# Optimization experiments

Measured on AMD Instinct MI355X. Metric: run time of the kernel, lower is better.

The kernel has to match this reference:

```python
import jax, jax.numpy as jnp
import numpy as np

EMBED_DIM = 192
NUM_HEADS = 4
HEAD_DIM = EMBED_DIM // NUM_HEADS
SCALE = HEAD_DIM ** -0.5


def setup_inputs() -> dict:
    key = jax.random.key(0)
    k_x, k_wqkv, k_bqkv, k_wp, k_bp = jax.random.split(key, 5)
    B, P, N, d = 8, 4, 1024, EMBED_DIM
    x = jax.random.normal(k_x, (B, P, N, d), dtype=jnp.float32)
    # torch Linear: y = x @ W.T + b, W shape [out, in]
    w_qkv = jax.random.normal(k_wqkv, (3 * d, d), dtype=jnp.float32) * (d ** -0.5)
    b_qkv = jax.random.normal(k_bqkv, (3 * d,), dtype=jnp.float32) * 0.02
    w_proj = jax.random.normal(k_wp, (d, d), dtype=jnp.float32) * (d ** -0.5)
    b_proj = jax.random.normal(k_bp, (d,), dtype=jnp.float32) * 0.02
    return {"x": x, "w_qkv": w_qkv, "b_qkv": b_qkv, "w_proj": w_proj, "b_proj": b_proj}


def reference(x, w_qkv, b_qkv, w_proj, b_proj):
    B, P, N, d = x.shape
    H, D = NUM_HEADS, HEAD_DIM
    qkv = jnp.einsum('bpnd,ed->bpne', x, w_qkv) + b_qkv  # [B,P,N,3d]
    q, k, v = jnp.split(qkv, 3, axis=-1)
    # split heads -> [B,P,H,N,D]
    split = lambda t: t.reshape(B, P, N, H, D).transpose(0, 1, 3, 2, 4)
    q, k, v = split(q), split(k), split(v)
    attn = jnp.einsum('bphnd,bphmd->bphnm', q, k) * SCALE
    attn = jax.nn.softmax(attn, axis=-1)
    z = jnp.einsum('bphnm,bphmd->bphnd', attn, v)
    z = z.transpose(0, 1, 3, 2, 4).reshape(B, P, N, H * D)
    z = jnp.einsum('bpnd,ed->bpne', z, w_proj) + b_proj
    return z
```

## Files before the change

### kernel.cpp

```cpp
#include <hip/hip_runtime.h>
#include <hip/hip_bf16.h>
#include <cstdint>
#include <cstddef>

typedef __attribute__((ext_vector_type(8))) short bf16x8;
typedef __attribute__((ext_vector_type(4))) float floatx4;
typedef __attribute__((ext_vector_type(16))) float floatx16;

#define SCALE_L2E 0.20823560929138437f

#define BPH 128
#define SEQ 1024
#define DMODEL 192
#define DHEAD 48
#define MROWS 32768
#define RESCALE_THR 11.5f

#define ZERO16 {0.f,0.f,0.f,0.f,0.f,0.f,0.f,0.f,0.f,0.f,0.f,0.f,0.f,0.f,0.f,0.f}

__device__ __forceinline__ unsigned short bfu(float f) {
    return __bfloat16_as_ushort(__float2bfloat16(f));
}
__device__ __forceinline__ unsigned pk2(float lo, float hi) {
    return (unsigned)bfu(lo) | ((unsigned)bfu(hi) << 16);
}

__global__ __launch_bounds__(256) void qkv_kernel(
    const float* __restrict__ x,
    const float* __restrict__ w_qkv,
    const float* __restrict__ b_qkv,
    unsigned short* __restrict__ q_ws,
    unsigned short* __restrict__ k_ws,
    unsigned short* __restrict__ vt_ws)
{
    __shared__ unsigned short a_lds[64 * 200];
    __shared__ unsigned short w_lds[64 * 200];
    const int t = threadIdx.x;
    const int m0 = blockIdx.x * 64;
    const int n0 = blockIdx.y * 64;

    #pragma unroll
    for (int i = 0; i < 12; ++i) {
        int idx = t + i * 256;
        int row = idx / 48, c4 = idx % 48;
        float4 v = *reinterpret_cast<const float4*>(x + (size_t)(m0 + row) * DMODEL + c4 * 4);
        unsigned short* dst = &a_lds[row * 200 + c4 * 4];
        dst[0] = bfu(v.x); dst[1] = bfu(v.y); dst[2] = bfu(v.z); dst[3] = bfu(v.w);
    }
    #pragma unroll
    for (int i = 0; i < 12; ++i) {
        int idx = t + i * 256;
        int row = idx / 48, c4 = idx % 48;
        float4 v = *reinterpret_cast<const float4*>(w_qkv + (size_t)(n0 + row) * DMODEL + c4 * 4);
        unsigned short* dst = &w_lds[row * 200 + c4 * 4];
        dst[0] = bfu(v.x); dst[1] = bfu(v.y); dst[2] = bfu(v.z); dst[3] = bfu(v.w);
    }
    __syncthreads();

    const int lane = t & 63, w = t >> 6;
    const int lrow = lane & 15, lhi = lane >> 4;

    floatx4 zf = {0.f, 0.f, 0.f, 0.f};
    floatx4 acc[4] = {zf, zf, zf, zf};

    #pragma unroll
    for (int ks = 0; ks < 6; ++ks) {
        bf16x8 af = *reinterpret_cast<const bf16x8*>(&a_lds[(w * 16 + lrow) * 200 + ks * 32 + lhi * 8]);
        #pragma unroll
        for (int cb = 0; cb < 4; ++cb) {
            bf16x8 bfr = *reinterpret_cast<const bf16x8*>(&w_lds[(cb * 16 + lrow) * 200 + ks * 32 + lhi * 8]);
            acc[cb] = __builtin_amdgcn_mfma_f32_16x16x32_bf16(af, bfr, acc[cb], 0, 0, 0);
        }
    }

    const int sec = n0 / 192;
    if (sec == 2) {
        __syncthreads();
        #pragma unroll
        for (int cb = 0; cb < 4; ++cb) {
            float bias = b_qkv[n0 + cb * 16 + lrow];
            #pragma unroll
            for (int r = 0; r < 4; ++r)
                a_lds[(cb * 16 + lrow) * 72 + (w * 16 + lhi * 4 + r)] = bfu(acc[cb][r] + bias);
        }
        __syncthreads();
        const int bp = m0 >> 10, nb = m0 & 1023;
        #pragma unroll
        for (int i = 0; i < 2; ++i) {
            int ch = t + i * 256;
            int c_local = ch >> 3, seg = ch & 7;
            int cc = n0 + c_local - 384;
            int h = cc / 48, dd = cc - h * 48;
            *reinterpret_cast<bf16x8*>(
                &vt_ws[((size_t)(bp * 4 + h) * DHEAD + dd) * SEQ + nb + seg * 8]) =
                *reinterpret_cast<const bf16x8*>(&a_lds[c_local * 72 + seg * 8]);
        }
    } else {
        #pragma unroll
        for (int cb = 0; cb < 4; ++cb) {
            int c = n0 + cb * 16 + lrow;
            int cc = c - sec * 192;
            int h = cc / 48, dd = cc - h * 48;
            float bias = b_qkv[c];
            #pragma unroll
            for (int r = 0; r < 4; ++r) {
                int m = m0 + w * 16 + lhi * 4 + r;
                float val = acc[cb][r] + bias;
                int bp = m >> 10, n = m & 1023;
                int bph = bp * 4 + h;
                if (sec == 0) {
                    q_ws[((size_t)bph * SEQ + n) * DHEAD + dd] = bfu(val * SCALE_L2E);
                } else {
                    k_ws[((size_t)bph * SEQ + n) * DHEAD + dd] = bfu(val);
                }
            }
        }
    }
}

__global__ __launch_bounds__(256, 4) void attn_kernel(
    const unsigned short* __restrict__ q_ws,
    const unsigned short* __restrict__ k_ws,
    const unsigned short* __restrict__ vt_ws,
    unsigned short* __restrict__ z_ws)
{
    const int t = threadIdx.x, lane = t & 63, w = t >> 6;
    const int q31 = lane & 31, hi = lane >> 5;
    const int d = blockIdx.x;
    const int bph = (d & 7) | ((d >> 6) << 3);
    const int qc = (d >> 3) & 7;
    const int q0 = qc * 128 + w * 32;
    const int bp = bph >> 2, h = bph & 3;

    bf16x8 qf[3];
    {
        const unsigned short* qp = q_ws + ((size_t)bph * SEQ + q0 + q31) * DHEAD + hi * 8;
        #pragma unroll
        for (int ks = 0; ks < 3; ++ks)
            qf[ks] = *reinterpret_cast<const bf16x8*>(qp + ks * 16);
    }

    const unsigned short* kp  = k_ws + ((size_t)bph * SEQ + q31) * DHEAD + hi * 8;
    const int vrow1 = (32 + q31 > 47) ? 47 : (32 + q31);
    const unsigned short* vp0 = vt_ws + ((size_t)bph * DHEAD + q31)  * (size_t)SEQ + hi * 8;
    const unsigned short* vp1 = vt_ws + ((size_t)bph * DHEAD + vrow1) * (size_t)SEQ + hi * 8;

    floatx16 oa0 = ZERO16, oa1 = ZERO16;
    float m_prev = -INFINITY, l_sum = 0.f;

    #pragma unroll 1
    for (int kt = 0; kt < 16; ++kt) {
        const int kt0 = kt * 64;

        const unsigned short* kpt = kp + (size_t)kt0 * DHEAD;
        bf16x8 kf[6], vf0[4], vf1[4];
        #pragma unroll
        for (int ks = 0; ks < 3; ++ks) {
            kf[ks]     = *reinterpret_cast<const bf16x8*>(kpt + ks * 16);
            kf[ks + 3] = *reinterpret_cast<const bf16x8*>(kpt + 32 * DHEAD + ks * 16);
        }
        #pragma unroll
        for (int ksv = 0; ksv < 4; ++ksv) {
            vf0[ksv] = *reinterpret_cast<const bf16x8*>(vp0 + kt0 + ksv * 16);
            vf1[ksv] = *reinterpret_cast<const bf16x8*>(vp1 + kt0 + ksv * 16);
        }

        floatx16 s0 = ZERO16, s1 = ZERO16;
        #pragma unroll
        for (int ks = 0; ks < 3; ++ks) {
            s0 = __builtin_amdgcn_mfma_f32_32x32x16_bf16(kf[ks],     qf[ks], s0, 0, 0, 0);
            s1 = __builtin_amdgcn_mfma_f32_32x32x16_bf16(kf[ks + 3], qf[ks], s1, 0, 0, 0);
        }

        float tmax = fmaxf(s0[0], s1[0]);
        #pragma unroll
        for (int r = 1; r < 16; ++r) tmax = fmaxf(tmax, fmaxf(s0[r], s1[r]));
        tmax = fmaxf(tmax, __shfl_xor(tmax, 32, 64));
        if (!__all((int)(tmax <= m_prev + RESCALE_THR))) {
            const float mnew = fmaxf(m_prev, tmax);
            const float scale = exp2f(m_prev - mnew);
            m_prev = mnew;
            l_sum *= scale;
            oa0 = oa0 * scale;
            oa1 = oa1 * scale;
        }
        const float mref = m_prev;

        float ts = 0.f;
        #pragma unroll
        for (int kvb = 0; kvb < 2; ++kvb) {
            unsigned W[8], X[8];
            #pragma unroll
            for (int u = 0; u < 8; ++u) {
                float e0 = __builtin_amdgcn_exp2f((kvb ? s1[2*u]   : s0[2*u])   - mref);
                float e1 = __builtin_amdgcn_exp2f((kvb ? s1[2*u+1] : s0[2*u+1]) - mref);
                ts += e0 + e1;
                W[u] = pk2(e0, e1);
                X[u] = __shfl_xor(W[u], 32, 64);
            }
            #pragma unroll
            for (int s = 0; s < 2; ++s) {
                const int a = s * 4;
                union { bf16x8 v; unsigned wd[4]; } pf;
                pf.wd[0] = hi ? X[a+2] : W[a];
                pf.wd[1] = hi ? X[a+3] : W[a+1];
                pf.wd[2] = hi ? W[a+2] : X[a];
                pf.wd[3] = hi ? W[a+3] : X[a+1];
                const int ksv = kvb * 2 + s;
                oa0 = __builtin_amdgcn_mfma_f32_32x32x16_bf16(vf0[ksv], pf.v, oa0, 0, 0, 0);
                oa1 = __builtin_amdgcn_mfma_f32_32x32x16_bf16(vf1[ksv], pf.v, oa1, 0, 0, 0);
            }
        }
        ts += __shfl_xor(ts, 32, 64);
        l_sum += ts;
    }

    const float inv = 1.0f / l_sum;
    unsigned* zp = reinterpret_cast<unsigned*>(
        z_ws + ((size_t)bp * SEQ + q0 + q31) * DMODEL + h * DHEAD);
    #pragma unroll
    for (int u = 0; u < 8; ++u) {
        int dd = 2 * (u & 1) + 8 * (u >> 1) + 4 * hi;
        zp[dd >> 1] = pk2(oa0[2*u] * inv, oa0[2*u+1] * inv);
    }
    #pragma unroll
    for (int u = 0; u < 4; ++u) {
        int dd = 32 + 2 * (u & 1) + 8 * (u >> 1) + 4 * hi;
        zp[dd >> 1] = pk2(oa1[2*u] * inv, oa1[2*u+1] * inv);
    }
}

__global__ __launch_bounds__(256) void proj_kernel(
    const unsigned short* __restrict__ z_ws,
    const float* __restrict__ w_proj,
    const float* __restrict__ b_proj,
    float* __restrict__ out)
{
    __shared__ unsigned short a_lds[64 * 200];
    __shared__ unsigned short w_lds[64 * 200];
    const int t = threadIdx.x;
    const int m0 = blockIdx.x * 64;
    const int n0 = blockIdx.y * 64;

    for (int i = t; i < 1536; i += 256) {
        int row = i / 24, c8 = i % 24;
        *reinterpret_cast<bf16x8*>(&a_lds[row * 200 + c8 * 8]) =
            *reinterpret_cast<const bf16x8*>(&z_ws[(size_t)(m0 + row) * DMODEL + c8 * 8]);
    }
    #pragma unroll
    for (int i = 0; i < 12; ++i) {
        int idx = t + i * 256;
        int row = idx / 48, c4 = idx % 48;
        float4 v = *reinterpret_cast<const float4*>(w_proj + (size_t)(n0 + row) * DMODEL + c4 * 4);
        unsigned short* dst = &w_lds[row * 200 + c4 * 4];
        dst[0] = bfu(v.x); dst[1] = bfu(v.y); dst[2] = bfu(v.z); dst[3] = bfu(v.w);
    }
    __syncthreads();

    const int lane = t & 63, w = t >> 6;
    const int lrow = lane & 15, lhi = lane >> 4;

    floatx4 zf = {0.f, 0.f, 0.f, 0.f};
    floatx4 acc[4] = {zf, zf, zf, zf};

    #pragma unroll
    for (int ks = 0; ks < 6; ++ks) {
        bf16x8 af = *reinterpret_cast<const bf16x8*>(&a_lds[(w * 16 + lrow) * 200 + ks * 32 + lhi * 8]);
        #pragma unroll
        for (int cb = 0; cb < 4; ++cb) {
            bf16x8 bfr = *reinterpret_cast<const bf16x8*>(&w_lds[(cb * 16 + lrow) * 200 + ks * 32 + lhi * 8]);
            acc[cb] = __builtin_amdgcn_mfma_f32_16x16x32_bf16(af, bfr, acc[cb], 0, 0, 0);
        }
    }

    #pragma unroll
    for (int cb = 0; cb < 4; ++cb) {
        int c = n0 + cb * 16 + lrow;
        float bias = b_proj[c];
        #pragma unroll
        for (int r = 0; r < 4; ++r) {
            int m = m0 + w * 16 + lhi * 4 + r;
            out[(size_t)m * DMODEL + c] = acc[cb][r] + bias;
        }
    }
}

extern "C" void kernel_launch(void* const* d_in, const int* in_sizes, int n_in,
                              void* d_out, int out_size, void* d_ws, size_t ws_size,
                              hipStream_t stream) {
    const float* x      = (const float*)d_in[0];
    const float* w_qkv  = (const float*)d_in[1];
    const float* b_qkv  = (const float*)d_in[2];
    const float* w_proj = (const float*)d_in[3];
    const float* b_proj = (const float*)d_in[4];
    float* out = (float*)d_out;

    unsigned short* q_ws  = (unsigned short*)d_ws;
    unsigned short* k_ws  = q_ws  + (size_t)BPH * SEQ * DHEAD;
    unsigned short* vt_ws = k_ws  + (size_t)BPH * SEQ * DHEAD;
    unsigned short* z_ws  = vt_ws + (size_t)BPH * DHEAD * SEQ;

    qkv_kernel<<<dim3(512, 9), 256, 0, stream>>>(x, w_qkv, b_qkv, q_ws, k_ws, vt_ws);
    attn_kernel<<<1024, 256, 0, stream>>>(q_ws, k_ws, vt_ws, z_ws);
    proj_kernel<<<dim3(512, 3), 256, 0, stream>>>(z_ws, w_proj, b_proj, out);
}
```

Measured before the change: 111.1 us.

## Stage K/V tiles through double-buffered LDS via async global-to-LDS loads

```diff
diff --git a/kernel.cpp b/kernel.cpp
--- a/kernel.cpp
+++ b/kernel.cpp
@@ -6,6 +6,7 @@
 typedef __attribute__((ext_vector_type(8))) short bf16x8;
 typedef __attribute__((ext_vector_type(4))) float floatx4;
 typedef __attribute__((ext_vector_type(16))) float floatx16;
+typedef __attribute__((ext_vector_type(2))) unsigned uintx2;
 
 #define SCALE_L2E 0.20823560929138437f
 
@@ -23,6 +24,12 @@
 }
 __device__ __forceinline__ unsigned pk2(float lo, float hi) {
     return (unsigned)bfu(lo) | ((unsigned)bfu(hi) << 16);
+}
+__device__ __forceinline__ void gload16(const unsigned short* g, unsigned short* l) {
+    __builtin_amdgcn_global_load_lds(
+        (const __attribute__((address_space(1))) unsigned int*)g,
+        (__attribute__((address_space(3))) unsigned int*)l,
+        16, 0, 0);
 }
 
 __global__ __launch_bounds__(256) void qkv_kernel(
@@ -44,16 +51,16 @@
         int idx = t + i * 256;
         int row = idx / 48, c4 = idx % 48;
         float4 v = *reinterpret_cast<const float4*>(x + (size_t)(m0 + row) * DMODEL + c4 * 4);
-        unsigned short* dst = &a_lds[row * 200 + c4 * 4];
-        dst[0] = bfu(v.x); dst[1] = bfu(v.y); dst[2] = bfu(v.z); dst[3] = bfu(v.w);
+        uintx2 p; p.x = pk2(v.x, v.y); p.y = pk2(v.z, v.w);
+        *reinterpret_cast<uintx2*>(&a_lds[row * 200 + c4 * 4]) = p;
     }
     #pragma unroll
     for (int i = 0; i < 12; ++i) {
         int idx = t + i * 256;
         int row = idx / 48, c4 = idx % 48;
         float4 v = *reinterpret_cast<const float4*>(w_qkv + (size_t)(n0 + row) * DMODEL + c4 * 4);
-        unsigned short* dst = &w_lds[row * 200 + c4 * 4];
-        dst[0] = bfu(v.x); dst[1] = bfu(v.y); dst[2] = bfu(v.z); dst[3] = bfu(v.w);
+        uintx2 p; p.x = pk2(v.x, v.y); p.y = pk2(v.z, v.w);
+        *reinterpret_cast<uintx2*>(&w_lds[row * 200 + c4 * 4]) = p;
     }
     __syncthreads();
 
@@ -124,6 +131,9 @@
     const unsigned short* __restrict__ vt_ws,
     unsigned short* __restrict__ z_ws)
 {
+    __shared__ unsigned short k_lds[2][384 * 8];
+    __shared__ unsigned short v_lds[2][384 * 8];
+
     const int t = threadIdx.x, lane = t & 63, w = t >> 6;
     const int q31 = lane & 31, hi = lane >> 5;
     const int d = blockIdx.x;
@@ -132,50 +142,85 @@
     const int q0 = qc * 128 + w * 32;
     const int bp = bph >> 2, h = bph & 3;
 
+    const size_t kbase = (size_t)bph * SEQ;
+    const size_t vbase = (size_t)bph * DHEAD;
+
+    const unsigned short* s0p = k_ws + (kbase + (t & 63)) * 48 + (t >> 6) * 8;
+    const unsigned short* s1p;
+    size_t step1;
+    int c1;
+    const bool c1k = (t < 128);
+    if (c1k) {
+        c1 = t + 256;
+        s1p = k_ws + (kbase + (c1 & 63)) * 48 + (c1 >> 6) * 8;
+        step1 = 48;
+    } else {
+        c1 = t - 128;
+        int vkhi = c1 / 48, dd = c1 - vkhi * 48;
+        s1p = vt_ws + (vbase + dd) * SEQ + vkhi * 8;
+        step1 = 1;
+    }
+    const int c2 = t + 128;
+    const int vkhi2 = c2 / 48, dd2 = c2 - vkhi2 * 48;
+    const unsigned short* s2p = vt_ws + (vbase + dd2) * SEQ + vkhi2 * 8;
+
     bf16x8 qf[3];
     {
-        const unsigned short* qp = q_ws + ((size_t)bph * SEQ + q0 + q31) * DHEAD + hi * 8;
+        const unsigned short* qp = q_ws + (kbase + q0 + q31) * DHEAD + hi * 8;
         #pragma unroll
         for (int ks = 0; ks < 3; ++ks)
             qf[ks] = *reinterpret_cast<const bf16x8*>(qp + ks * 16);
     }
 
-    const unsigned short* kp  = k_ws + ((size_t)bph * SEQ + q31) * DHEAD + hi * 8;
-    const int vrow1 = (32 + q31 > 47) ? 47 : (32 + q31);
-    const unsigned short* vp0 = vt_ws + ((size_t)bph * DHEAD + q31)  * (size_t)SEQ + hi * 8;
-    const unsigned short* vp1 = vt_ws + ((size_t)bph * DHEAD + vrow1) * (size_t)SEQ + hi * 8;
+    const int vrow1m = (32 + q31 > 47) ? 47 : (32 + q31);
 
     floatx16 oa0 = ZERO16, oa1 = ZERO16;
     float m_prev = -INFINITY, l_sum = 0.f;
 
+    gload16(s0p, &k_lds[0][t * 8]);
+    gload16(s1p, c1k ? &k_lds[0][c1 * 8] : &v_lds[0][c1 * 8]);
+    gload16(s2p, &v_lds[0][c2 * 8]);
+    __syncthreads();
+
     #pragma unroll 1
     for (int kt = 0; kt < 16; ++kt) {
-        const int kt0 = kt * 64;
-
-        const unsigned short* kpt = kp + (size_t)kt0 * DHEAD;
+        const int cur = kt & 1;
+        if (kt < 15) {
+            const size_t kt0n = (size_t)(kt + 1) * 64;
+            gload16(s0p + kt0n * 48,   &k_lds[cur ^ 1][t * 8]);
+            gload16(s1p + kt0n * step1, c1k ? &k_lds[cur ^ 1][c1 * 8] : &v_lds[cur ^ 1][c1 * 8]);
+            gload16(s2p + kt0n,        &v_lds[cur ^ 1][c2 * 8]);
+        }
+
+        const unsigned short* kb = k_lds[cur];
+        const unsigned short* vb = v_lds[cur];
+
         bf16x8 kf[6], vf0[4], vf1[4];
         #pragma unroll
         for (int ks = 0; ks < 3; ++ks) {
-            kf[ks]     = *reinterpret_cast<const bf16x8*>(kpt + ks * 16);
-            kf[ks + 3] = *reinterpret_cast<const bf16x8*>(kpt + 32 * DHEAD + ks * 16);
+            kf[ks]     = *reinterpret_cast<const bf16x8*>(&kb[((ks * 2 + hi) * 64 + q31) * 8]);
+            kf[ks + 3] = *reinterpret_cast<const bf16x8*>(&kb[((ks * 2 + hi) * 64 + q31 + 32) * 8]);
         }
         #pragma unroll
         for (int ksv = 0; ksv < 4; ++ksv) {
-            vf0[ksv] = *reinterpret_cast<const bf16x8*>(vp0 + kt0 + ksv * 16);
-            vf1[ksv] = *reinterpret_cast<const bf16x8*>(vp1 + kt0 + ksv * 16);
+            vf0[ksv] = *reinterpret_cast<const bf16x8*>(&vb[((ksv * 2 + hi) * 48 + q31) * 8]);
+            vf1[ksv] = *reinterpret_cast<const bf16x8*>(&vb[((ksv * 2 + hi) * 48 + vrow1m) * 8]);
         }
 
         floatx16 s0 = ZERO16, s1 = ZERO16;
+        __builtin_amdgcn_s_setprio(1);
         #pragma unroll
         for (int ks = 0; ks < 3; ++ks) {
             s0 = __builtin_amdgcn_mfma_f32_32x32x16_bf16(kf[ks],     qf[ks], s0, 0, 0, 0);
             s1 = __builtin_amdgcn_mfma_f32_32x32x16_bf16(kf[ks + 3], qf[ks], s1, 0, 0, 0);
         }
+        __builtin_amdgcn_s_setprio(0);
 
         float tmax = fmaxf(s0[0], s1[0]);
         #pragma unroll
         for (int r = 1; r < 16; ++r) tmax = fmaxf(tmax, fmaxf(s0[r], s1[r]));
         tmax = fmaxf(tmax, __shfl_xor(tmax, 32, 64));
+
         if (!__all((int)(tmax <= m_prev + RESCALE_THR))) {
             const float mnew = fmaxf(m_prev, tmax);
             const float scale = exp2f(m_prev - mnew);
@@ -187,6 +232,8 @@
         const float mref = m_prev;
 
         float ts = 0.f;
+        union U { bf16x8 v; unsigned wd[4]; };
+        __builtin_amdgcn_s_setprio(1);
         #pragma unroll
         for (int kvb = 0; kvb < 2; ++kvb) {
             unsigned W[8], X[8];
@@ -201,7 +248,7 @@
             #pragma unroll
             for (int s = 0; s < 2; ++s) {
                 const int a = s * 4;
-                union { bf16x8 v; unsigned wd[4]; } pf;
+                U pf;
                 pf.wd[0] = hi ? X[a+2] : W[a];
                 pf.wd[1] = hi ? X[a+3] : W[a+1];
                 pf.wd[2] = hi ? W[a+2] : X[a];
@@ -211,8 +258,11 @@
                 oa1 = __builtin_amdgcn_mfma_f32_32x32x16_bf16(vf1[ksv], pf.v, oa1, 0, 0, 0);
             }
         }
+        __builtin_amdgcn_s_setprio(0);
         ts += __shfl_xor(ts, 32, 64);
         l_sum += ts;
+
+        __syncthreads();
     }
 
     const float inv = 1.0f / l_sum;
@@ -252,8 +302,8 @@
         int idx = t + i * 256;
         int row = idx / 48, c4 = idx % 48;
         float4 v = *reinterpret_cast<const float4*>(w_proj + (size_t)(n0 + row) * DMODEL + c4 * 4);
-        unsigned short* dst = &w_lds[row * 200 + c4 * 4];
-        dst[0] = bfu(v.x); dst[1] = bfu(v.y); dst[2] = bfu(v.z); dst[3] = bfu(v.w);
+        uintx2 p; p.x = pk2(v.x, v.y); p.y = pk2(v.z, v.w);
+        *reinterpret_cast<uintx2*>(&w_lds[row * 200 + c4 * 4]) = p;
     }
     __syncthreads();
 
```

New measurement: 119.1 us. 1.07x slower.

## Use P-as-A-operand 32x32x8 MFMA with blocked V layout to drop shuffles

Applied to the files above, without the earlier changes.

```diff
diff --git a/kernel.cpp b/kernel.cpp
--- a/kernel.cpp
+++ b/kernel.cpp
@@ -4,8 +4,10 @@
 #include <cstddef>
 
 typedef __attribute__((ext_vector_type(8))) short bf16x8;
+typedef __attribute__((ext_vector_type(4))) short bf16x4;
 typedef __attribute__((ext_vector_type(4))) float floatx4;
 typedef __attribute__((ext_vector_type(16))) float floatx16;
+typedef __attribute__((ext_vector_type(2))) unsigned uintx2;
 
 #define SCALE_L2E 0.20823560929138437f
 
@@ -15,6 +17,7 @@
 #define DHEAD 48
 #define MROWS 32768
 #define RESCALE_THR 11.5f
+#define VSTRIDE 49152
 
 #define ZERO16 {0.f,0.f,0.f,0.f,0.f,0.f,0.f,0.f,0.f,0.f,0.f,0.f,0.f,0.f,0.f,0.f}
 
@@ -24,6 +27,17 @@
 __device__ __forceinline__ unsigned pk2(float lo, float hi) {
     return (unsigned)bfu(lo) | ((unsigned)bfu(hi) << 16);
 }
+
+#if __has_builtin(__builtin_amdgcn_mfma_f32_32x32x8bf16_1k)
+__device__ __forceinline__ floatx16 mfma8(bf16x4 a, bf16x4 b, floatx16 c) {
+    return __builtin_amdgcn_mfma_f32_32x32x8bf16_1k(a, b, c, 0, 0, 0);
+}
+#else
+__device__ __forceinline__ floatx16 mfma8(bf16x4 a, bf16x4 b, floatx16 c) {
+    asm("v_mfma_f32_32x32x8_bf16 %0, %1, %2, %0" : "+v"(c) : "v"(a), "v"(b));
+    return c;
+}
+#endif
 
 __global__ __launch_bounds__(256) void qkv_kernel(
     const float* __restrict__ x,
@@ -31,7 +45,7 @@
     const float* __restrict__ b_qkv,
     unsigned short* __restrict__ q_ws,
     unsigned short* __restrict__ k_ws,
-    unsigned short* __restrict__ vt_ws)
+    unsigned short* __restrict__ v2_ws)
 {
     __shared__ unsigned short a_lds[64 * 200];
     __shared__ unsigned short w_lds[64 * 200];
@@ -44,16 +58,16 @@
         int idx = t + i * 256;
         int row = idx / 48, c4 = idx % 48;
         float4 v = *reinterpret_cast<const float4*>(x + (size_t)(m0 + row) * DMODEL + c4 * 4);
-        unsigned short* dst = &a_lds[row * 200 + c4 * 4];
-        dst[0] = bfu(v.x); dst[1] = bfu(v.y); dst[2] = bfu(v.z); dst[3] = bfu(v.w);
+        uintx2 p; p.x = pk2(v.x, v.y); p.y = pk2(v.z, v.w);
+        *reinterpret_cast<uintx2*>(&a_lds[row * 200 + c4 * 4]) = p;
     }
     #pragma unroll
     for (int i = 0; i < 12; ++i) {
         int idx = t + i * 256;
         int row = idx / 48, c4 = idx % 48;
         float4 v = *reinterpret_cast<const float4*>(w_qkv + (size_t)(n0 + row) * DMODEL + c4 * 4);
-        unsigned short* dst = &w_lds[row * 200 + c4 * 4];
-        dst[0] = bfu(v.x); dst[1] = bfu(v.y); dst[2] = bfu(v.z); dst[3] = bfu(v.w);
+        uintx2 p; p.x = pk2(v.x, v.y); p.y = pk2(v.z, v.w);
+        *reinterpret_cast<uintx2*>(&w_lds[row * 200 + c4 * 4]) = p;
     }
     __syncthreads();
 
@@ -92,7 +106,7 @@
             int cc = n0 + c_local - 384;
             int h = cc / 48, dd = cc - h * 48;
             *reinterpret_cast<bf16x8*>(
-                &vt_ws[((size_t)(bp * 4 + h) * DHEAD + dd) * SEQ + nb + seg * 8]) =
+                &v2_ws[(size_t)(bp * 4 + h) * VSTRIDE + (size_t)(nb / 8 + seg) * 384 + dd * 8]) =
                 *reinterpret_cast<const bf16x8*>(&a_lds[c_local * 72 + seg * 8]);
         }
     } else {
@@ -121,7 +135,7 @@
 __global__ __launch_bounds__(256, 4) void attn_kernel(
     const unsigned short* __restrict__ q_ws,
     const unsigned short* __restrict__ k_ws,
-    const unsigned short* __restrict__ vt_ws,
+    const unsigned short* __restrict__ v2_ws,
     unsigned short* __restrict__ z_ws)
 {
     const int t = threadIdx.x, lane = t & 63, w = t >> 6;
@@ -140,93 +154,96 @@
             qf[ks] = *reinterpret_cast<const bf16x8*>(qp + ks * 16);
     }
 
-    const unsigned short* kp  = k_ws + ((size_t)bph * SEQ + q31) * DHEAD + hi * 8;
-    const int vrow1 = (32 + q31 > 47) ? 47 : (32 + q31);
-    const unsigned short* vp0 = vt_ws + ((size_t)bph * DHEAD + q31)  * (size_t)SEQ + hi * 8;
-    const unsigned short* vp1 = vt_ws + ((size_t)bph * DHEAD + vrow1) * (size_t)SEQ + hi * 8;
+    const unsigned short* kp = k_ws + ((size_t)bph * SEQ + q31) * DHEAD + hi * 8;
+    const int dB = 32 + (q31 < 16 ? q31 : 15);
+    const unsigned short* vpA = v2_ws + (size_t)bph * VSTRIDE + q31 * 8 + hi * 4;
+    const unsigned short* vpB = v2_ws + (size_t)bph * VSTRIDE + dB  * 8 + hi * 4;
 
     floatx16 oa0 = ZERO16, oa1 = ZERO16;
     float m_prev = -INFINITY, l_sum = 0.f;
 
     #pragma unroll 1
     for (int kt = 0; kt < 16; ++kt) {
-        const int kt0 = kt * 64;
-
-        const unsigned short* kpt = kp + (size_t)kt0 * DHEAD;
-        bf16x8 kf[6], vf0[4], vf1[4];
+        const unsigned short* kpt = kp + (size_t)kt * 64 * DHEAD;
+        bf16x8 kf[6];
         #pragma unroll
         for (int ks = 0; ks < 3; ++ks) {
             kf[ks]     = *reinterpret_cast<const bf16x8*>(kpt + ks * 16);
             kf[ks + 3] = *reinterpret_cast<const bf16x8*>(kpt + 32 * DHEAD + ks * 16);
         }
-        #pragma unroll
-        for (int ksv = 0; ksv < 4; ++ksv) {
-            vf0[ksv] = *reinterpret_cast<const bf16x8*>(vp0 + kt0 + ksv * 16);
-            vf1[ksv] = *reinterpret_cast<const bf16x8*>(vp1 + kt0 + ksv * 16);
+        bf16x4 vA[8], vB[8];
+        const size_t vto = (size_t)kt * 3072;
+        #pragma unroll
+        for (int j = 0; j < 8; ++j) {
+            vA[j] = *reinterpret_cast<const bf16x4*>(vpA + vto + j * 384);
+            vB[j] = *reinterpret_cast<const bf16x4*>(vpB + vto + j * 384);
         }
 
         floatx16 s0 = ZERO16, s1 = ZERO16;
+        __builtin_amdgcn_s_setprio(1);
         #pragma unroll
         for (int ks = 0; ks < 3; ++ks) {
             s0 = __builtin_amdgcn_mfma_f32_32x32x16_bf16(kf[ks],     qf[ks], s0, 0, 0, 0);
             s1 = __builtin_amdgcn_mfma_f32_32x32x16_bf16(kf[ks + 3], qf[ks], s1, 0, 0, 0);
         }
+        __builtin_amdgcn_s_setprio(0);
 
         float tmax = fmaxf(s0[0], s1[0]);
         #pragma unroll
         for (int r = 1; r < 16; ++r) tmax = fmaxf(tmax, fmaxf(s0[r], s1[r]));
         tmax = fmaxf(tmax, __shfl_xor(tmax, 32, 64));
+
         if (!__all((int)(tmax <= m_prev + RESCALE_THR))) {
             const float mnew = fmaxf(m_prev, tmax);
             const float scale = exp2f(m_prev - mnew);
             m_prev = mnew;
             l_sum *= scale;
-            oa0 = oa0 * scale;
-            oa1 = oa1 * scale;
+            #pragma unroll
+            for (int r = 0; r < 16; ++r) {
+                float sr = __shfl(scale, (r & 3) + 8 * (r >> 2) + 4 * hi, 64);
+                oa0[r] *= sr;
+                oa1[r] *= sr;
+            }
         }
         const float mref = m_prev;
 
         float ts = 0.f;
-        #pragma unroll
-        for (int kvb = 0; kvb < 2; ++kvb) {
-            unsigned W[8], X[8];
-            #pragma unroll
-            for (int u = 0; u < 8; ++u) {
-                float e0 = __builtin_amdgcn_exp2f((kvb ? s1[2*u]   : s0[2*u])   - mref);
-                float e1 = __builtin_amdgcn_exp2f((kvb ? s1[2*u+1] : s0[2*u+1]) - mref);
-                ts += e0 + e1;
-                W[u] = pk2(e0, e1);
-                X[u] = __shfl_xor(W[u], 32, 64);
+        union AU { bf16x4 v; unsigned u[2]; };
+        __builtin_amdgcn_s_setprio(1);
+        #pragma unroll
+        for (int j = 0; j < 8; ++j) {
+            float e0, e1, e2, e3;
+            if (j < 4) {
+                e0 = __builtin_amdgcn_exp2f(s0[4*j]   - mref);
+                e1 = __builtin_amdgcn_exp2f(s0[4*j+1] - mref);
+                e2 = __builtin_amdgcn_exp2f(s0[4*j+2] - mref);
+                e3 = __builtin_amdgcn_exp2f(s0[4*j+3] - mref);
+            } else {
+                e0 = __builtin_amdgcn_exp2f(s1[4*(j-4)]   - mref);
+                e1 = __builtin_amdgcn_exp2f(s1[4*(j-4)+1] - mref);
+                e2 = __builtin_amdgcn_exp2f(s1[4*(j-4)+2] - mref);
+                e3 = __builtin_amdgcn_exp2f(s1[4*(j-4)+3] - mref);
             }
-            #pragma unroll
-            for (int s = 0; s < 2; ++s) {
-                const int a = s * 4;
-                union { bf16x8 v; unsigned wd[4]; } pf;
-                pf.wd[0] = hi ? X[a+2] : W[a];
-                pf.wd[1] = hi ? X[a+3] : W[a+1];
-                pf.wd[2] = hi ? W[a+2] : X[a];
-                pf.wd[3] = hi ? W[a+3] : X[a+1];
-                const int ksv = kvb * 2 + s;
-                oa0 = __builtin_amdgcn_mfma_f32_32x32x16_bf16(vf0[ksv], pf.v, oa0, 0, 0, 0);
-                oa1 = __builtin_amdgcn_mfma_f32_32x32x16_bf16(vf1[ksv], pf.v, oa1, 0, 0, 0);
-            }
-        }
+            ts += (e0 + e1) + (e2 + e3);
+            AU aj;
+            aj.u[0] = pk2(e0, e1);
+            aj.u[1] = pk2(e2, e3);
+            oa0 = mfma8(aj.v, vA[j], oa0);
+            oa1 = mfma8(aj.v, vB[j], oa1);
+        }
+        __builtin_amdgcn_s_setprio(0);
         ts += __shfl_xor(ts, 32, 64);
         l_sum += ts;
     }
 
     const float inv = 1.0f / l_sum;
-    unsigned* zp = reinterpret_cast<unsigned*>(
-        z_ws + ((size_t)bp * SEQ + q0 + q31) * DMODEL + h * DHEAD);
-    #pragma unroll
-    for (int u = 0; u < 8; ++u) {
-        int dd = 2 * (u & 1) + 8 * (u >> 1) + 4 * hi;
-        zp[dd >> 1] = pk2(oa0[2*u] * inv, oa0[2*u+1] * inv);
-    }
-    #pragma unroll
-    for (int u = 0; u < 4; ++u) {
-        int dd = 32 + 2 * (u & 1) + 8 * (u >> 1) + 4 * hi;
-        zp[dd >> 1] = pk2(oa1[2*u] * inv, oa1[2*u+1] * inv);
+    #pragma unroll
+    for (int r = 0; r < 16; ++r) {
+        const int qr = (r & 3) + 8 * (r >> 2) + 4 * hi;
+        const float ir = __shfl(inv, qr, 64);
+        unsigned short* zr = z_ws + ((size_t)bp * SEQ + q0 + qr) * DMODEL + h * DHEAD;
+        zr[q31] = bfu(oa0[r] * ir);
+        if (q31 < 16) zr[32 + q31] = bfu(oa1[r] * ir);
     }
 }
 
@@ -252,8 +269,8 @@
         int idx = t + i * 256;
         int row = idx / 48, c4 = idx % 48;
         float4 v = *reinterpret_cast<const float4*>(w_proj + (size_t)(n0 + row) * DMODEL + c4 * 4);
-        unsigned short* dst = &w_lds[row * 200 + c4 * 4];
-        dst[0] = bfu(v.x); dst[1] = bfu(v.y); dst[2] = bfu(v.z); dst[3] = bfu(v.w);
+        uintx2 p; p.x = pk2(v.x, v.y); p.y = pk2(v.z, v.w);
+        *reinterpret_cast<uintx2*>(&w_lds[row * 200 + c4 * 4]) = p;
     }
     __syncthreads();
 
@@ -297,10 +314,10 @@
 
     unsigned short* q_ws  = (unsigned short*)d_ws;
     unsigned short* k_ws  = q_ws  + (size_t)BPH * SEQ * DHEAD;
-    unsigned short* vt_ws = k_ws  + (size_t)BPH * SEQ * DHEAD;
-    unsigned short* z_ws  = vt_ws + (size_t)BPH * DHEAD * SEQ;
-
-    qkv_kernel<<<dim3(512, 9), 256, 0, stream>>>(x, w_qkv, b_qkv, q_ws, k_ws, vt_ws);
-    attn_kernel<<<1024, 256, 0, stream>>>(q_ws, k_ws, vt_ws, z_ws);
+    unsigned short* v2_ws = k_ws  + (size_t)BPH * SEQ * DHEAD;
+    unsigned short* z_ws  = v2_ws + (size_t)BPH * VSTRIDE;
+
+    qkv_kernel<<<dim3(512, 9), 256, 0, stream>>>(x, w_qkv, b_qkv, q_ws, k_ws, v2_ws);
+    attn_kernel<<<1024, 256, 0, stream>>>(q_ws, k_ws, v2_ws, z_ws);
     proj_kernel<<<dim3(512, 3), 256, 0, stream>>>(z_ws, w_proj, b_proj, out);
 }
```

Measured after the change: 116.4 us. +4.8%, slower.
